# Kernel optimization log

Hardware: AMD Instinct MI355X
Metric: run time of the kernel (lower is better)

Reference implementation:

```python
import jax, jax.numpy as jnp
import numpy as np

N, E, B, D, L = 50000, 1600000, 128, 64, 5
BN_EPS = 1e-5

def _bn(x, g, b, m, v):
    # eval-mode BatchNorm1d with running stats
    return (x - m) * jax.lax.rsqrt(v + BN_EPS) * g + b

def setup_inputs() -> dict:
    key = jax.random.key(0)
    ks = iter(jax.random.split(key, 64))
    w = 1.0 / np.sqrt(D)
    def nrm(shape, s):
        return jax.random.normal(next(ks), shape, jnp.float32) * s
    def var(shape):
        return jax.random.uniform(next(ks), shape, jnp.float32) + 0.5
    inp = {
        "x": nrm((N, D), 1.0),
        "lin_W": nrm((D, D), w), "lin_b": nrm((D,), w),
        "eps": jnp.zeros((L,), jnp.float32),
        "gin_W1": nrm((L, D, D), w), "gin_b1": nrm((L, D), w),
        "gin_bn_g": jnp.ones((L, D), jnp.float32), "gin_bn_b": jnp.zeros((L, D), jnp.float32),
        "gin_bn_m": nrm((L, D), 0.1), "gin_bn_v": var((L, D)),
        "gin_W2": nrm((L, D, D), w), "gin_b2": nrm((L, D), w),
        "bn_g": jnp.ones((L, D), jnp.float32), "bn_b": jnp.zeros((L, D), jnp.float32),
        "bn_m": nrm((L, D), 0.1), "bn_v": var((L, D)),
        "vn_emb": jnp.zeros((D,), jnp.float32),  # init constant 0 per source
        "vn_W1": nrm((L - 1, D, D), w), "vn_b1": nrm((L - 1, D), w),
        "vn_bn1_g": jnp.ones((L - 1, D), jnp.float32), "vn_bn1_b": jnp.zeros((L - 1, D), jnp.float32),
        "vn_bn1_m": nrm((L - 1, D), 0.1), "vn_bn1_v": var((L - 1, D)),
        "vn_W2": nrm((L - 1, D, D), w), "vn_b2": nrm((L - 1, D), w),
        "vn_bn2_g": jnp.ones((L - 1, D), jnp.float32), "vn_bn2_b": jnp.zeros((L - 1, D), jnp.float32),
        "vn_bn2_m": nrm((L - 1, D), 0.1), "vn_bn2_v": var((L - 1, D)),
        "src": jax.random.randint(next(ks), (E,), 0, N, jnp.int32),
        "dst": jax.random.randint(next(ks), (E,), 0, N, jnp.int32),
        "batch_id": jnp.sort(jax.random.randint(next(ks), (N,), 0, B, jnp.int32)),
    }
    return inp

def reference(x, lin_W, lin_b, eps, gin_W1, gin_b1, gin_bn_g, gin_bn_b, gin_bn_m, gin_bn_v,
              gin_W2, gin_b2, bn_g, bn_b, bn_m, bn_v, vn_emb,
              vn_W1, vn_b1, vn_bn1_g, vn_bn1_b, vn_bn1_m, vn_bn1_v,
              vn_W2, vn_b2, vn_bn2_g, vn_bn2_b, vn_bn2_m, vn_bn2_v,
              src, dst, batch_id):
    n = x.shape[0]
    h = x @ lin_W + lin_b                       # input linear [N, D]
    h_list = [h]
    vn = jnp.broadcast_to(vn_emb, (B, D))       # per-graph virtual node [B, D]
    for l in range(L):
        h_list[l] = h_list[l] + vn[batch_id]    # virtual-node broadcast to nodes
        hl = h_list[l]
        # GINConv: sum over incoming edges of relu(src feature)
        agg = jax.ops.segment_sum(jax.nn.relu(hl[src]), dst, num_segments=n)
        z = (1.0 + eps[l]) * hl + agg
        z = z @ gin_W1[l] + gin_b1[l]
        z = jax.nn.relu(_bn(z, gin_bn_g[l], gin_bn_b[l], gin_bn_m[l], gin_bn_v[l]))
        z = z @ gin_W2[l] + gin_b2[l]
        z = _bn(z, bn_g[l], bn_b[l], bn_m[l], bn_v[l])  # outer batchnorm
        if l != L - 1:
            z = jax.nn.relu(z)                  # dropout is identity in eval mode
        h_list.append(z)
        if l < L - 1:
            # sum-pool nodes per graph, update virtual node via MLP
            vt = jax.ops.segment_sum(hl, batch_id, num_segments=B) + vn
            vt = vt @ vn_W1[l] + vn_b1[l]
            vt = jax.nn.relu(_bn(vt, vn_bn1_g[l], vn_bn1_b[l], vn_bn1_m[l], vn_bn1_v[l]))
            vt = vt @ vn_W2[l] + vn_b2[l]
            vn = jax.nn.relu(_bn(vt, vn_bn2_g[l], vn_bn2_b[l], vn_bn2_m[l], vn_bn2_v[l]))
    # JK='sum' in the source sums h_list[0..num_layers-1] (excludes final entry)
    out = h_list[0]
    for l in range(1, L):
        out = out + h_list[l]
    return out
```

## Files before the change

kernel.cpp:

```cpp
#include <hip/hip_runtime.h>

#define N_NODES 50000
#define N_EDGES 1600000
#define NB 128
#define GB 782
#define AGG_HALF (N_NODES / 4)
#define CAP 80
#define NODE_RANGE 6250
#define EDGE_BLOCKS 6250
#define INIT_BLOCKS 32

__device__ __forceinline__ unsigned short f2bf(float f) {
    unsigned u = __float_as_uint(f);
    unsigned r = (u + 0x7FFFu + ((u >> 16) & 1u)) >> 16;
    return (unsigned short)r;
}
__device__ __forceinline__ float bf2f(unsigned short u) {
    return __uint_as_float(((unsigned)u) << 16);
}

__global__ __launch_bounds__(256) void k_build(
    const int* __restrict__ src, const int* __restrict__ dst,
    int* __restrict__ cnt, unsigned short* __restrict__ csr_src,
    const float* __restrict__ vn_emb, float* __restrict__ pooled) {
    int bid = blockIdx.x;
    if (bid >= EDGE_BLOCKS * 8) {
        int t = (bid - EDGE_BLOCKS * 8) * 256 + threadIdx.x;
        pooled[t] = vn_emb[t & 63];
        return;
    }
    int range = bid & 7;
    int e = (bid >> 3) * 256 + threadIdx.x;
    int d = dst[e];
    if (d / NODE_RANGE != range) return;
    int pos = atomicAdd(&cnt[d], 1);
    if (pos < CAP) csr_src[(size_t)d * CAP + pos] = (unsigned short)src[e];
}

__global__ __launch_bounds__(256) void k_lin_pre(
    const float* __restrict__ in, const float* __restrict__ W,
    const float* __restrict__ bias, const float* __restrict__ vn_emb,
    const int* __restrict__ batch_id,
    float* __restrict__ h, float* __restrict__ out,
    unsigned short* __restrict__ rbuf, float* __restrict__ pooled) {
    __shared__ float sW[64 * 64];
    __shared__ float sIn[64 * 68];
    int tid = threadIdx.x;
    int row0 = blockIdx.x * 64;

    const float4* W4 = (const float4*)W;
#pragma unroll
    for (int i = 0; i < 4; ++i) ((float4*)sW)[tid + 256 * i] = W4[tid + 256 * i];
    const float4* in4 = (const float4*)in;
#pragma unroll
    for (int i = 0; i < 4; ++i) {
        int idx = tid + 256 * i;
        int r = idx >> 4, j = idx & 15;
        float4 val = make_float4(0.f, 0.f, 0.f, 0.f);
        if (row0 + r < N_NODES) val = in4[(size_t)(row0 + r) * 16 + j];
        ((float4*)(sIn + r * 68))[j] = val;
    }
    __syncthreads();

    int c4 = (tid & 15) * 4;
    int rl = (tid >> 4) * 4;
    float acc[4][4] = {{0.f}};
#pragma unroll 8
    for (int k = 0; k < 64; ++k) {
        float4 wv = *(const float4*)(sW + k * 64 + c4);
        float a0 = sIn[(rl + 0) * 68 + k];
        float a1 = sIn[(rl + 1) * 68 + k];
        float a2 = sIn[(rl + 2) * 68 + k];
        float a3 = sIn[(rl + 3) * 68 + k];
        acc[0][0] += a0 * wv.x; acc[0][1] += a0 * wv.y; acc[0][2] += a0 * wv.z; acc[0][3] += a0 * wv.w;
        acc[1][0] += a1 * wv.x; acc[1][1] += a1 * wv.y; acc[1][2] += a1 * wv.z; acc[1][3] += a1 * wv.w;
        acc[2][0] += a2 * wv.x; acc[2][1] += a2 * wv.y; acc[2][2] += a2 * wv.z; acc[2][3] += a2 * wv.w;
        acc[3][0] += a3 * wv.x; acc[3][1] += a3 * wv.y; acc[3][2] += a3 * wv.z; acc[3][3] += a3 * wv.w;
    }
    float shf[4];
#pragma unroll
    for (int j = 0; j < 4; ++j) shf[j] = bias[c4 + j] + vn_emb[c4 + j];

    int lane = tid & 63;
    int wave = tid >> 6;
    int wr0 = row0 + wave * 16;
    bool full = (wr0 + 15 < N_NODES);
    bool fast = full && (batch_id[wr0] == batch_id[wr0 + 15]);
    float4 pacc = make_float4(0.f, 0.f, 0.f, 0.f);
#pragma unroll
    for (int r = 0; r < 4; ++r) {
        int row = row0 + rl + r;
        if (row >= N_NODES) continue;
        float4 v;
        v.x = acc[r][0] + shf[0];
        v.y = acc[r][1] + shf[1];
        v.z = acc[r][2] + shf[2];
        v.w = acc[r][3] + shf[3];
        *(float4*)(h + (size_t)row * 64 + c4) = v;
        *(float4*)(out + (size_t)row * 64 + c4) = v;
        ushort4 rb;
        rb.x = f2bf(fmaxf(v.x, 0.f)); rb.y = f2bf(fmaxf(v.y, 0.f));
        rb.z = f2bf(fmaxf(v.z, 0.f)); rb.w = f2bf(fmaxf(v.w, 0.f));
        *(ushort4*)(rbuf + (size_t)(c4 >> 5) * ((size_t)N_NODES * 32)
                    + (size_t)row * 32 + (c4 & 31)) = rb;
        if (fast) {
            pacc.x += v.x; pacc.y += v.y; pacc.z += v.z; pacc.w += v.w;
        } else {
            int b = batch_id[row];
            atomicAdd(&pooled[b * 64 + c4 + 0], v.x);
            atomicAdd(&pooled[b * 64 + c4 + 1], v.y);
            atomicAdd(&pooled[b * 64 + c4 + 2], v.z);
            atomicAdd(&pooled[b * 64 + c4 + 3], v.w);
        }
    }
    if (fast) {
        pacc.x += __shfl_xor(pacc.x, 16); pacc.x += __shfl_xor(pacc.x, 32);
        pacc.y += __shfl_xor(pacc.y, 16); pacc.y += __shfl_xor(pacc.y, 32);
        pacc.z += __shfl_xor(pacc.z, 16); pacc.z += __shfl_xor(pacc.z, 32);
        pacc.w += __shfl_xor(pacc.w, 16); pacc.w += __shfl_xor(pacc.w, 32);
        if ((lane >> 4) == 0) {
            int b = batch_id[wr0];
            atomicAdd(&pooled[b * 64 + c4 + 0], pacc.x);
            atomicAdd(&pooled[b * 64 + c4 + 1], pacc.y);
            atomicAdd(&pooled[b * 64 + c4 + 2], pacc.z);
            atomicAdd(&pooled[b * 64 + c4 + 3], pacc.w);
        }
    }
}

__global__ __launch_bounds__(256) void k_agg(
    const float* __restrict__ h, const unsigned short* __restrict__ rbuf,
    const int* __restrict__ cnt, const unsigned short* __restrict__ csr_src,
    float* __restrict__ agg, const float* __restrict__ eps, int l) {
    int wave = threadIdx.x >> 6, lane = threadIdx.x & 63;
    int bx = blockIdx.x;
    int half = (bx >= AGG_HALF) ? 1 : 0;
    int node = (bx - half * AGG_HALF) * 4 + wave;
    const uint4* tab4 = (const uint4*)(rbuf + (size_t)half * ((size_t)N_NODES * 32));
    int deg = cnt[node]; if (deg > CAP) deg = CAP;
    const unsigned short* rowp = csr_src + (size_t)node * CAP;
    int g = lane >> 2;
    int f4 = lane & 3;
    float aLo[4] = {0.f, 0.f, 0.f, 0.f};
    float aHi[4] = {0.f, 0.f, 0.f, 0.f};
    for (int base = 0; base < deg; base += 64) {
        int e = base + lane;
        int s = (e < deg) ? (int)rowp[e] : 0;
        int c = deg - base; if (c > 64) c = 64;
        for (int t = 0; t < c; t += 16) {
            int idx = t + g;
            int sj = __shfl(s, (idx < c) ? idx : t);
            if (idx < c) {
                uint4 u = tab4[(size_t)sj * 4 + f4];
                aLo[0] += __uint_as_float(u.x << 16);
                aHi[0] += __uint_as_float(u.x & 0xFFFF0000u);
                aLo[1] += __uint_as_float(u.y << 16);
                aHi[1] += __uint_as_float(u.y & 0xFFFF0000u);
                aLo[2] += __uint_as_float(u.z << 16);
                aHi[2] += __uint_as_float(u.z & 0xFFFF0000u);
                aLo[3] += __uint_as_float(u.w << 16);
                aHi[3] += __uint_as_float(u.w & 0xFFFF0000u);
            }
        }
    }
#pragma unroll
    for (int k = 0; k < 4; ++k) {
        aLo[k] += __shfl_xor(aLo[k], 4);  aHi[k] += __shfl_xor(aHi[k], 4);
        aLo[k] += __shfl_xor(aLo[k], 8);  aHi[k] += __shfl_xor(aHi[k], 8);
        aLo[k] += __shfl_xor(aLo[k], 16); aHi[k] += __shfl_xor(aHi[k], 16);
        aLo[k] += __shfl_xor(aLo[k], 32); aHi[k] += __shfl_xor(aHi[k], 32);
    }
    if (g == 0) {
        int c = half * 32 + f4 * 8;
        float e1 = 1.0f + eps[l];
        const float* hp = h + (size_t)node * 64 + c;
        float4 h0 = *(const float4*)(hp);
        float4 h1 = *(const float4*)(hp + 4);
        float4 o0, o1;
        o0.x = e1 * h0.x + aLo[0]; o0.y = e1 * h0.y + aHi[0];
        o0.z = e1 * h0.z + aLo[1]; o0.w = e1 * h0.w + aHi[1];
        o1.x = e1 * h1.x + aLo[2]; o1.y = e1 * h1.y + aHi[2];
        o1.z = e1 * h1.z + aLo[3]; o1.w = e1 * h1.w + aHi[3];
        float* op = agg + (size_t)node * 64 + c;
        *(float4*)(op) = o0;
        *(float4*)(op + 4) = o1;
    }
}

__global__ __launch_bounds__(256) void k_gin(
    const float* __restrict__ in,
    const float* __restrict__ W1, const float* __restrict__ b1,
    const float* __restrict__ g1, const float* __restrict__ be1,
    const float* __restrict__ m1, const float* __restrict__ v1,
    const float* __restrict__ W2, const float* __restrict__ b2,
    const float* __restrict__ g2, const float* __restrict__ be2,
    const float* __restrict__ m2, const float* __restrict__ v2,
    const float* __restrict__ vn, const int* __restrict__ batch_id,
    float* __restrict__ h, float* __restrict__ out,
    unsigned short* __restrict__ rbuf, float* __restrict__ pooled,
    int last) {
    __shared__ float sW[64 * 64];
    __shared__ float sIn[64 * 68];
    int tid = threadIdx.x;
    int row0 = blockIdx.x * 64;

#pragma unroll
    for (int i = 0; i < 4; ++i) ((float4*)sW)[tid + 256 * i] = ((const float4*)W1)[tid + 256 * i];
    const float4* in4 = (const float4*)in;
#pragma unroll
    for (int i = 0; i < 4; ++i) {
        int idx = tid + 256 * i;
        int r = idx >> 4, j = idx & 15;
        float4 val = make_float4(0.f, 0.f, 0.f, 0.f);
        if (row0 + r < N_NODES) val = in4[(size_t)(row0 + r) * 16 + j];
        ((float4*)(sIn + r * 68))[j] = val;
    }
    __syncthreads();

    int c4 = (tid & 15) * 4;
    int rl = (tid >> 4) * 4;
    float acc[4][4] = {{0.f}};
#pragma unroll 8
    for (int k = 0; k < 64; ++k) {
        float4 wv = *(const float4*)(sW + k * 64 + c4);
        float a0 = sIn[(rl + 0) * 68 + k];
        float a1 = sIn[(rl + 1) * 68 + k];
        float a2 = sIn[(rl + 2) * 68 + k];
        float a3 = sIn[(rl + 3) * 68 + k];
        acc[0][0] += a0 * wv.x; acc[0][1] += a0 * wv.y; acc[0][2] += a0 * wv.z; acc[0][3] += a0 * wv.w;
        acc[1][0] += a1 * wv.x; acc[1][1] += a1 * wv.y; acc[1][2] += a1 * wv.z; acc[1][3] += a1 * wv.w;
        acc[2][0] += a2 * wv.x; acc[2][1] += a2 * wv.y; acc[2][2] += a2 * wv.z; acc[2][3] += a2 * wv.w;
        acc[3][0] += a3 * wv.x; acc[3][1] += a3 * wv.y; acc[3][2] += a3 * wv.z; acc[3][3] += a3 * wv.w;
    }
    float scl[4], shf[4];
#pragma unroll
    for (int j = 0; j < 4; ++j) {
        int c = c4 + j;
        float sc = g1[c] * rsqrtf(v1[c] + 1e-5f);
        scl[j] = sc;
        shf[j] = be1[c] - m1[c] * sc + b1[c] * sc;
    }
    __syncthreads();
#pragma unroll
    for (int i = 0; i < 4; ++i) {
        float4 z;
        z.x = fmaxf(acc[i][0] * scl[0] + shf[0], 0.f);
        z.y = fmaxf(acc[i][1] * scl[1] + shf[1], 0.f);
        z.z = fmaxf(acc[i][2] * scl[2] + shf[2], 0.f);
        z.w = fmaxf(acc[i][3] * scl[3] + shf[3], 0.f);
        *(float4*)(sIn + (rl + i) * 68 + c4) = z;
    }
#pragma unroll
    for (int i = 0; i < 4; ++i) ((float4*)sW)[tid + 256 * i] = ((const float4*)W2)[tid + 256 * i];
    __syncthreads();

    float acc2[4][4] = {{0.f}};
#pragma unroll 8
    for (int k = 0; k < 64; ++k) {
        float4 wv = *(const float4*)(sW + k * 64 + c4);
        float a0 = sIn[(rl + 0) * 68 + k];
        float a1 = sIn[(rl + 1) * 68 + k];
        float a2 = sIn[(rl + 2) * 68 + k];
        float a3 = sIn[(rl + 3) * 68 + k];
        acc2[0][0] += a0 * wv.x; acc2[0][1] += a0 * wv.y; acc2[0][2] += a0 * wv.z; acc2[0][3] += a0 * wv.w;
        acc2[1][0] += a1 * wv.x; acc2[1][1] += a1 * wv.y; acc2[1][2] += a1 * wv.z; acc2[1][3] += a1 * wv.w;
        acc2[2][0] += a2 * wv.x; acc2[2][1] += a2 * wv.y; acc2[2][2] += a2 * wv.z; acc2[2][3] += a2 * wv.w;
        acc2[3][0] += a3 * wv.x; acc2[3][1] += a3 * wv.y; acc2[3][2] += a3 * wv.z; acc2[3][3] += a3 * wv.w;
    }
#pragma unroll
    for (int j = 0; j < 4; ++j) {
        int c = c4 + j;
        float sc = g2[c] * rsqrtf(v2[c] + 1e-5f);
        scl[j] = sc;
        shf[j] = be2[c] - m2[c] * sc + b2[c] * sc;
    }

    int lane = tid & 63;
    int wave = tid >> 6;
    int wr0 = row0 + wave * 16;
    bool full = (wr0 + 15 < N_NODES);
    bool fast = (!last) && full && (batch_id[wr0] == batch_id[wr0 + 15]);
    float4 pacc = make_float4(0.f, 0.f, 0.f, 0.f);
#pragma unroll
    for (int r = 0; r < 4; ++r) {
        int row = row0 + rl + r;
        if (row >= N_NODES) continue;
        int b = batch_id[row];
        float4 vv = *(const float4*)(vn + b * 64 + c4);
        float4 v;
        v.x = fmaxf(acc2[r][0] * scl[0] + shf[0], 0.f) + vv.x;
        v.y = fmaxf(acc2[r][1] * scl[1] + shf[1], 0.f) + vv.y;
        v.z = fmaxf(acc2[r][2] * scl[2] + shf[2], 0.f) + vv.z;
        v.w = fmaxf(acc2[r][3] * scl[3] + shf[3], 0.f) + vv.w;
        float4 o = *(const float4*)(out + (size_t)row * 64 + c4);
        o.x += v.x; o.y += v.y; o.z += v.z; o.w += v.w;
        *(float4*)(out + (size_t)row * 64 + c4) = o;
        if (!last) {
            *(float4*)(h + (size_t)row * 64 + c4) = v;
            ushort4 rb;
            rb.x = f2bf(fmaxf(v.x, 0.f)); rb.y = f2bf(fmaxf(v.y, 0.f));
            rb.z = f2bf(fmaxf(v.z, 0.f)); rb.w = f2bf(fmaxf(v.w, 0.f));
            *(ushort4*)(rbuf + (size_t)(c4 >> 5) * ((size_t)N_NODES * 32)
                        + (size_t)row * 32 + (c4 & 31)) = rb;
            if (fast) {
                pacc.x += v.x; pacc.y += v.y; pacc.z += v.z; pacc.w += v.w;
            } else {
                atomicAdd(&pooled[b * 64 + c4 + 0], v.x);
                atomicAdd(&pooled[b * 64 + c4 + 1], v.y);
                atomicAdd(&pooled[b * 64 + c4 + 2], v.z);
                atomicAdd(&pooled[b * 64 + c4 + 3], v.w);
            }
        }
    }
    if (fast) {
        pacc.x += __shfl_xor(pacc.x, 16); pacc.x += __shfl_xor(pacc.x, 32);
        pacc.y += __shfl_xor(pacc.y, 16); pacc.y += __shfl_xor(pacc.y, 32);
        pacc.z += __shfl_xor(pacc.z, 16); pacc.z += __shfl_xor(pacc.z, 32);
        pacc.w += __shfl_xor(pacc.w, 16); pacc.w += __shfl_xor(pacc.w, 32);
        if ((lane >> 4) == 0) {
            int b = batch_id[wr0];
            atomicAdd(&pooled[b * 64 + c4 + 0], pacc.x);
            atomicAdd(&pooled[b * 64 + c4 + 1], pacc.y);
            atomicAdd(&pooled[b * 64 + c4 + 2], pacc.z);
            atomicAdd(&pooled[b * 64 + c4 + 3], pacc.w);
        }
    }
}

__global__ __launch_bounds__(1024) void k_vnmlp(
    const float* __restrict__ pooled_in,
    const float* __restrict__ W1, const float* __restrict__ b1,
    const float* __restrict__ g1, const float* __restrict__ be1,
    const float* __restrict__ m1, const float* __restrict__ v1,
    const float* __restrict__ W2, const float* __restrict__ b2,
    const float* __restrict__ g2, const float* __restrict__ be2,
    const float* __restrict__ m2, const float* __restrict__ v2,
    float* __restrict__ vn_out, float* __restrict__ pooled_out) {
    __shared__ float sP[128 * 68];
    __shared__ float sW[64 * 64];
    int tid = threadIdx.x;

    ((float4*)sW)[tid] = ((const float4*)W1)[tid];
#pragma unroll
    for (int i = 0; i < 2; ++i) {
        int idx = tid + 1024 * i;
        int r = idx >> 4, j = idx & 15;
        ((float4*)(sP + r * 68))[j] = ((const float4*)pooled_in)[idx];
    }
    __syncthreads();

    int c4 = (tid & 15) * 4, rg = tid >> 4;
    float acc[2][4] = {{0.f}};
#pragma unroll 8
    for (int k = 0; k < 64; ++k) {
        float4 w = *(const float4*)(sW + k * 64 + c4);
#pragma unroll
        for (int i = 0; i < 2; ++i) {
            float a = sP[(rg * 2 + i) * 68 + k];
            acc[i][0] += a * w.x; acc[i][1] += a * w.y;
            acc[i][2] += a * w.z; acc[i][3] += a * w.w;
        }
    }
    float scl[4], shf[4];
#pragma unroll
    for (int j = 0; j < 4; ++j) {
        int c = c4 + j;
        float sc = g1[c] * rsqrtf(v1[c] + 1e-5f);
        scl[j] = sc;
        shf[j] = be1[c] - m1[c] * sc + b1[c] * sc;
    }
    __syncthreads();
#pragma unroll
    for (int i = 0; i < 2; ++i) {
        float4 z;
        z.x = fmaxf(acc[i][0] * scl[0] + shf[0], 0.f);
        z.y = fmaxf(acc[i][1] * scl[1] + shf[1], 0.f);
        z.z = fmaxf(acc[i][2] * scl[2] + shf[2], 0.f);
        z.w = fmaxf(acc[i][3] * scl[3] + shf[3], 0.f);
        *(float4*)(sP + (rg * 2 + i) * 68 + c4) = z;
    }
    ((float4*)sW)[tid] = ((const float4*)W2)[tid];
    __syncthreads();

    float acc2[2][4] = {{0.f}};
#pragma unroll 8
    for (int k = 0; k < 64; ++k) {
        float4 w = *(const float4*)(sW + k * 64 + c4);
#pragma unroll
        for (int i = 0; i < 2; ++i) {
            float a = sP[(rg * 2 + i) * 68 + k];
            acc2[i][0] += a * w.x; acc2[i][1] += a * w.y;
            acc2[i][2] += a * w.z; acc2[i][3] += a * w.w;
        }
    }
#pragma unroll
    for (int j = 0; j < 4; ++j) {
        int c = c4 + j;
        float sc = g2[c] * rsqrtf(v2[c] + 1e-5f);
        scl[j] = sc;
        shf[j] = be2[c] - m2[c] * sc + b2[c] * sc;
    }
#pragma unroll
    for (int i = 0; i < 2; ++i) {
        int row = rg * 2 + i;
        float4 o;
        o.x = fmaxf(acc2[i][0] * scl[0] + shf[0], 0.f);
        o.y = fmaxf(acc2[i][1] * scl[1] + shf[1], 0.f);
        o.z = fmaxf(acc2[i][2] * scl[2] + shf[2], 0.f);
        o.w = fmaxf(acc2[i][3] * scl[3] + shf[3], 0.f);
        *(float4*)(vn_out + row * 64 + c4) = o;
        *(float4*)(pooled_out + row * 64 + c4) = o;
    }
}

extern "C" void kernel_launch(void* const* d_in, const int* in_sizes, int n_in,
                              void* d_out, int out_size, void* d_ws, size_t ws_size,
                              hipStream_t stream) {
    const float* x      = (const float*)d_in[0];
    const float* lin_W  = (const float*)d_in[1];
    const float* lin_b  = (const float*)d_in[2];
    const float* eps    = (const float*)d_in[3];
    const float* gin_W1 = (const float*)d_in[4];
    const float* gin_b1 = (const float*)d_in[5];
    const float* gbn_g  = (const float*)d_in[6];
    const float* gbn_b  = (const float*)d_in[7];
    const float* gbn_m  = (const float*)d_in[8];
    const float* gbn_v  = (const float*)d_in[9];
    const float* gin_W2 = (const float*)d_in[10];
    const float* gin_b2 = (const float*)d_in[11];
    const float* bn_g   = (const float*)d_in[12];
    const float* bn_b   = (const float*)d_in[13];
    const float* bn_m   = (const float*)d_in[14];
    const float* bn_v   = (const float*)d_in[15];
    const float* vn_emb = (const float*)d_in[16];
    const float* vn_W1  = (const float*)d_in[17];
    const float* vn_b1  = (const float*)d_in[18];
    const float* v1g    = (const float*)d_in[19];
    const float* v1b    = (const float*)d_in[20];
    const float* v1m    = (const float*)d_in[21];
    const float* v1v    = (const float*)d_in[22];
    const float* vn_W2  = (const float*)d_in[23];
    const float* vn_b2  = (const float*)d_in[24];
    const float* v2g    = (const float*)d_in[25];
    const float* v2b    = (const float*)d_in[26];
    const float* v2m    = (const float*)d_in[27];
    const float* v2v    = (const float*)d_in[28];
    const int* src      = (const int*)d_in[29];
    const int* dst      = (const int*)d_in[30];
    const int* batch_id = (const int*)d_in[31];
    float* out = (float*)d_out;

    float* h      = (float*)d_ws;
    float* agg    = h   + (size_t)N_NODES * 64;
    unsigned short* rbuf = (unsigned short*)(agg + (size_t)N_NODES * 64);
    float* vn     = (float*)(rbuf + (size_t)N_NODES * 64);
    float* pooled = vn  + (size_t)NB * 64;
    int*   cnt    = (int*)(pooled + (size_t)NB * 64);
    unsigned short* csr_src = (unsigned short*)(cnt + N_NODES);

    hipMemsetAsync(cnt, 0, N_NODES * sizeof(int), stream);
    k_build<<<EDGE_BLOCKS * 8 + INIT_BLOCKS, 256, 0, stream>>>(src, dst, cnt, csr_src,
                                                               vn_emb, pooled);

    k_lin_pre<<<GB, 256, 0, stream>>>(x, lin_W, lin_b, vn_emb, batch_id,
                                      h, out, rbuf, pooled);

    for (int l = 0; l < 4; ++l) {
        k_vnmlp<<<1, 1024, 0, stream>>>(pooled,
                                        vn_W1 + l * 4096, vn_b1 + l * 64,
                                        v1g + l * 64, v1b + l * 64, v1m + l * 64, v1v + l * 64,
                                        vn_W2 + l * 4096, vn_b2 + l * 64,
                                        v2g + l * 64, v2b + l * 64, v2m + l * 64, v2v + l * 64,
                                        vn, pooled);
        k_agg<<<2 * AGG_HALF, 256, 0, stream>>>(h, rbuf, cnt, csr_src, agg, eps, l);
        k_gin<<<GB, 256, 0, stream>>>(agg,
                                      gin_W1 + l * 4096, gin_b1 + l * 64,
                                      gbn_g + l * 64, gbn_b + l * 64,
                                      gbn_m + l * 64, gbn_v + l * 64,
                                      gin_W2 + l * 4096, gin_b2 + l * 64,
                                      bn_g + l * 64, bn_b + l * 64,
                                      bn_m + l * 64, bn_v + l * 64,
                                      vn, batch_id, h, out, rbuf, pooled,
                                      l == 3);
    }
}
```

Before: 542.4 us.

## Fuse neighbor aggregation into GIN MLP kernel with double-buffered bf16 relu table

Removes the separate aggregation kernel. Each GIN block now gathers neighbor bf16 relu features for its own 64 rows straight into shared memory before the MLP, so the fp32 agg buffer is no longer written and read back. The relu table switches from two half-width planes to one row-major 64-wide layout, giving each neighbor a single contiguous 128-byte gather. The table is ping-ponged between two buffers because blocks now read it while other blocks write the next layer's copy. The trade-off is much less parallelism for the latency-bound gather: each wave walks 16 nodes serially, on only 782 blocks.

```diff
diff --git a/kernel.cpp b/kernel.cpp
--- a/kernel.cpp
+++ b/kernel.cpp
@@ -4,7 +4,6 @@
 #define N_EDGES 1600000
 #define NB 128
 #define GB 782
-#define AGG_HALF (N_NODES / 4)
 #define CAP 80
 #define NODE_RANGE 6250
 #define EDGE_BLOCKS 6250
@@ -14,9 +13,6 @@
     unsigned u = __float_as_uint(f);
     unsigned r = (u + 0x7FFFu + ((u >> 16) & 1u)) >> 16;
     return (unsigned short)r;
-}
-__device__ __forceinline__ float bf2f(unsigned short u) {
-    return __uint_as_float(((unsigned)u) << 16);
 }
 
 __global__ __launch_bounds__(256) void k_build(
@@ -101,8 +97,7 @@
         ushort4 rb;
         rb.x = f2bf(fmaxf(v.x, 0.f)); rb.y = f2bf(fmaxf(v.y, 0.f));
         rb.z = f2bf(fmaxf(v.z, 0.f)); rb.w = f2bf(fmaxf(v.w, 0.f));
-        *(ushort4*)(rbuf + (size_t)(c4 >> 5) * ((size_t)N_NODES * 32)
-                    + (size_t)row * 32 + (c4 & 31)) = rb;
+        *(ushort4*)(rbuf + (size_t)row * 64 + c4) = rb;
         if (fast) {
             pacc.x += v.x; pacc.y += v.y; pacc.z += v.z; pacc.w += v.w;
         } else {
@@ -128,67 +123,10 @@
     }
 }
 
-__global__ __launch_bounds__(256) void k_agg(
-    const float* __restrict__ h, const unsigned short* __restrict__ rbuf,
+__global__ __launch_bounds__(256) void k_gin(
+    const float* __restrict__ h_in, const float* __restrict__ eps, int l,
     const int* __restrict__ cnt, const unsigned short* __restrict__ csr_src,
-    float* __restrict__ agg, const float* __restrict__ eps, int l) {
-    int wave = threadIdx.x >> 6, lane = threadIdx.x & 63;
-    int bx = blockIdx.x;
-    int half = (bx >= AGG_HALF) ? 1 : 0;
-    int node = (bx - half * AGG_HALF) * 4 + wave;
-    const uint4* tab4 = (const uint4*)(rbuf + (size_t)half * ((size_t)N_NODES * 32));
-    int deg = cnt[node]; if (deg > CAP) deg = CAP;
-    const unsigned short* rowp = csr_src + (size_t)node * CAP;
-    int g = lane >> 2;
-    int f4 = lane & 3;
-    float aLo[4] = {0.f, 0.f, 0.f, 0.f};
-    float aHi[4] = {0.f, 0.f, 0.f, 0.f};
-    for (int base = 0; base < deg; base += 64) {
-        int e = base + lane;
-        int s = (e < deg) ? (int)rowp[e] : 0;
-        int c = deg - base; if (c > 64) c = 64;
-        for (int t = 0; t < c; t += 16) {
-            int idx = t + g;
-            int sj = __shfl(s, (idx < c) ? idx : t);
-            if (idx < c) {
-                uint4 u = tab4[(size_t)sj * 4 + f4];
-                aLo[0] += __uint_as_float(u.x << 16);
-                aHi[0] += __uint_as_float(u.x & 0xFFFF0000u);
-                aLo[1] += __uint_as_float(u.y << 16);
-                aHi[1] += __uint_as_float(u.y & 0xFFFF0000u);
-                aLo[2] += __uint_as_float(u.z << 16);
-                aHi[2] += __uint_as_float(u.z & 0xFFFF0000u);
-                aLo[3] += __uint_as_float(u.w << 16);
-                aHi[3] += __uint_as_float(u.w & 0xFFFF0000u);
-            }
-        }
-    }
-#pragma unroll
-    for (int k = 0; k < 4; ++k) {
-        aLo[k] += __shfl_xor(aLo[k], 4);  aHi[k] += __shfl_xor(aHi[k], 4);
-        aLo[k] += __shfl_xor(aLo[k], 8);  aHi[k] += __shfl_xor(aHi[k], 8);
-        aLo[k] += __shfl_xor(aLo[k], 16); aHi[k] += __shfl_xor(aHi[k], 16);
-        aLo[k] += __shfl_xor(aLo[k], 32); aHi[k] += __shfl_xor(aHi[k], 32);
-    }
-    if (g == 0) {
-        int c = half * 32 + f4 * 8;
-        float e1 = 1.0f + eps[l];
-        const float* hp = h + (size_t)node * 64 + c;
-        float4 h0 = *(const float4*)(hp);
-        float4 h1 = *(const float4*)(hp + 4);
-        float4 o0, o1;
-        o0.x = e1 * h0.x + aLo[0]; o0.y = e1 * h0.y + aHi[0];
-        o0.z = e1 * h0.z + aLo[1]; o0.w = e1 * h0.w + aHi[1];
-        o1.x = e1 * h1.x + aLo[2]; o1.y = e1 * h1.y + aHi[2];
-        o1.z = e1 * h1.z + aLo[3]; o1.w = e1 * h1.w + aHi[3];
-        float* op = agg + (size_t)node * 64 + c;
-        *(float4*)(op) = o0;
-        *(float4*)(op + 4) = o1;
-    }
-}
-
-__global__ __launch_bounds__(256) void k_gin(
-    const float* __restrict__ in,
+    const unsigned short* __restrict__ rbuf_in,
     const float* __restrict__ W1, const float* __restrict__ b1,
     const float* __restrict__ g1, const float* __restrict__ be1,
     const float* __restrict__ m1, const float* __restrict__ v1,
@@ -197,23 +135,73 @@
     const float* __restrict__ m2, const float* __restrict__ v2,
     const float* __restrict__ vn, const int* __restrict__ batch_id,
     float* __restrict__ h, float* __restrict__ out,
-    unsigned short* __restrict__ rbuf, float* __restrict__ pooled,
+    unsigned short* __restrict__ rbuf_out, float* __restrict__ pooled,
     int last) {
     __shared__ float sW[64 * 64];
     __shared__ float sIn[64 * 68];
     int tid = threadIdx.x;
     int row0 = blockIdx.x * 64;
+    int lane = tid & 63;
+    int wave = tid >> 6;
 
 #pragma unroll
     for (int i = 0; i < 4; ++i) ((float4*)sW)[tid + 256 * i] = ((const float4*)W1)[tid + 256 * i];
-    const float4* in4 = (const float4*)in;
-#pragma unroll
-    for (int i = 0; i < 4; ++i) {
-        int idx = tid + 256 * i;
-        int r = idx >> 4, j = idx & 15;
-        float4 val = make_float4(0.f, 0.f, 0.f, 0.f);
-        if (row0 + r < N_NODES) val = in4[(size_t)(row0 + r) * 16 + j];
-        ((float4*)(sIn + r * 68))[j] = val;
+
+    {
+        int g = lane >> 3, f4 = lane & 7;
+        float e1 = 1.0f + eps[l];
+        const uint4* tab4 = (const uint4*)rbuf_in;
+#pragma unroll 1
+        for (int i = 0; i < 16; ++i) {
+            int row = row0 + wave * 16 + i;
+            float aL0 = 0.f, aH0 = 0.f, aL1 = 0.f, aH1 = 0.f;
+            float aL2 = 0.f, aH2 = 0.f, aL3 = 0.f, aH3 = 0.f;
+            if (row < N_NODES) {
+                int deg = cnt[row]; if (deg > CAP) deg = CAP;
+                const unsigned short* rowp = csr_src + (size_t)row * CAP;
+                for (int base = 0; base < deg; base += 64) {
+                    int e = base + lane;
+                    int s = (e < deg) ? (int)rowp[e] : 0;
+                    int c = deg - base; if (c > 64) c = 64;
+                    for (int t = 0; t < c; t += 8) {
+                        int idx = t + g;
+                        int sj = __shfl(s, (idx < c) ? idx : t);
+                        if (idx < c) {
+                            uint4 u = tab4[(size_t)sj * 8 + f4];
+                            aL0 += __uint_as_float(u.x << 16); aH0 += __uint_as_float(u.x & 0xFFFF0000u);
+                            aL1 += __uint_as_float(u.y << 16); aH1 += __uint_as_float(u.y & 0xFFFF0000u);
+                            aL2 += __uint_as_float(u.z << 16); aH2 += __uint_as_float(u.z & 0xFFFF0000u);
+                            aL3 += __uint_as_float(u.w << 16); aH3 += __uint_as_float(u.w & 0xFFFF0000u);
+                        }
+                    }
+                }
+            }
+#pragma unroll
+            for (int off = 8; off < 64; off <<= 1) {
+                aL0 += __shfl_xor(aL0, off); aH0 += __shfl_xor(aH0, off);
+                aL1 += __shfl_xor(aL1, off); aH1 += __shfl_xor(aH1, off);
+                aL2 += __shfl_xor(aL2, off); aH2 += __shfl_xor(aH2, off);
+                aL3 += __shfl_xor(aL3, off); aH3 += __shfl_xor(aH3, off);
+            }
+            if (g == 0) {
+                float* sp = sIn + (wave * 16 + i) * 68 + f4 * 8;
+                if (row < N_NODES) {
+                    const float* hp = h_in + (size_t)row * 64 + f4 * 8;
+                    float4 h0 = *(const float4*)hp;
+                    float4 h1 = *(const float4*)(hp + 4);
+                    float4 o0, o1;
+                    o0.x = e1 * h0.x + aL0; o0.y = e1 * h0.y + aH0;
+                    o0.z = e1 * h0.z + aL1; o0.w = e1 * h0.w + aH1;
+                    o1.x = e1 * h1.x + aL2; o1.y = e1 * h1.y + aH2;
+                    o1.z = e1 * h1.z + aL3; o1.w = e1 * h1.w + aH3;
+                    *(float4*)sp = o0;
+                    *(float4*)(sp + 4) = o1;
+                } else {
+                    *(float4*)sp = make_float4(0.f, 0.f, 0.f, 0.f);
+                    *(float4*)(sp + 4) = make_float4(0.f, 0.f, 0.f, 0.f);
+                }
+            }
+        }
     }
     __syncthreads();
 
@@ -275,8 +263,6 @@
         shf[j] = be2[c] - m2[c] * sc + b2[c] * sc;
     }
 
-    int lane = tid & 63;
-    int wave = tid >> 6;
     int wr0 = row0 + wave * 16;
     bool full = (wr0 + 15 < N_NODES);
     bool fast = (!last) && full && (batch_id[wr0] == batch_id[wr0 + 15]);
@@ -300,8 +286,7 @@
             ushort4 rb;
             rb.x = f2bf(fmaxf(v.x, 0.f)); rb.y = f2bf(fmaxf(v.y, 0.f));
             rb.z = f2bf(fmaxf(v.z, 0.f)); rb.w = f2bf(fmaxf(v.w, 0.f));
-            *(ushort4*)(rbuf + (size_t)(c4 >> 5) * ((size_t)N_NODES * 32)
-                        + (size_t)row * 32 + (c4 & 31)) = rb;
+            *(ushort4*)(rbuf_out + (size_t)row * 64 + c4) = rb;
             if (fast) {
                 pacc.x += v.x; pacc.y += v.y; pacc.z += v.z; pacc.w += v.w;
             } else {
@@ -451,9 +436,9 @@
     float* out = (float*)d_out;
 
     float* h      = (float*)d_ws;
-    float* agg    = h   + (size_t)N_NODES * 64;
-    unsigned short* rbuf = (unsigned short*)(agg + (size_t)N_NODES * 64);
-    float* vn     = (float*)(rbuf + (size_t)N_NODES * 64);
+    unsigned short* rbufA = (unsigned short*)(h + (size_t)N_NODES * 64);
+    unsigned short* rbufB = rbufA + (size_t)N_NODES * 64;
+    float* vn     = (float*)(rbufB + (size_t)N_NODES * 64);
     float* pooled = vn  + (size_t)NB * 64;
     int*   cnt    = (int*)(pooled + (size_t)NB * 64);
     unsigned short* csr_src = (unsigned short*)(cnt + N_NODES);
@@ -463,24 +448,25 @@
                                                                vn_emb, pooled);
 
     k_lin_pre<<<GB, 256, 0, stream>>>(x, lin_W, lin_b, vn_emb, batch_id,
-                                      h, out, rbuf, pooled);
+                                      h, out, rbufA, pooled);
 
     for (int l = 0; l < 4; ++l) {
+        unsigned short* rin  = (l & 1) ? rbufB : rbufA;
+        unsigned short* rout = (l & 1) ? rbufA : rbufB;
         k_vnmlp<<<1, 1024, 0, stream>>>(pooled,
                                         vn_W1 + l * 4096, vn_b1 + l * 64,
                                         v1g + l * 64, v1b + l * 64, v1m + l * 64, v1v + l * 64,
                                         vn_W2 + l * 4096, vn_b2 + l * 64,
                                         v2g + l * 64, v2b + l * 64, v2m + l * 64, v2v + l * 64,
                                         vn, pooled);
-        k_agg<<<2 * AGG_HALF, 256, 0, stream>>>(h, rbuf, cnt, csr_src, agg, eps, l);
-        k_gin<<<GB, 256, 0, stream>>>(agg,
+        k_gin<<<GB, 256, 0, stream>>>(h, eps, l, cnt, csr_src, rin,
                                       gin_W1 + l * 4096, gin_b1 + l * 64,
                                       gbn_g + l * 64, gbn_b + l * 64,
                                       gbn_m + l * 64, gbn_v + l * 64,
                                       gin_W2 + l * 4096, gin_b2 + l * 64,
                                       bn_g + l * 64, bn_b + l * 64,
                                       bn_m + l * 64, bn_v + l * 64,
-                                      vn, batch_id, h, out, rbuf, pooled,
+                                      vn, batch_id, h, out, rout, pooled,
                                       l == 3);
     }
 }
```

After: 545.3 us. No clear change (+0.5%).
